# Optimization experiments

Hardware: AMD Instinct MI355X
Metric: run time of the kernel (lower is better)

Reference implementation:

```python
import jax, jax.numpy as jnp
import numpy as np

D_IN = 1024
D_OUT = 1024
SEQ = 4096


def setup_inputs() -> dict:
    key = jax.random.key(0)
    k0, k1, k2, k3 = jax.random.split(key, 4)
    inputs = jax.random.normal(k0, (SEQ, D_IN), dtype=jnp.float32)
    # original uses torch.rand (uniform [0,1)) for weights
    W_q = jax.random.uniform(k1, (D_IN, D_OUT), dtype=jnp.float32)
    W_k = jax.random.uniform(k2, (D_IN, D_OUT), dtype=jnp.float32)
    W_v = jax.random.uniform(k3, (D_IN, D_OUT), dtype=jnp.float32)
    return {"inputs": inputs, "W_q": W_q, "W_k": W_k, "W_v": W_v}


def reference(inputs, W_q, W_k, W_v):
    queries = inputs @ W_q            # [S, d_out]
    keys = inputs @ W_k               # [S, d_out]
    values = inputs @ W_v             # [S, d_out]
    d_k = keys.shape[-1]
    scale = 1.0 / jnp.sqrt(jnp.asarray(d_k, dtype=queries.dtype))
    attn_scores = queries @ keys.T    # [S, S]
    attn_weights = jax.nn.softmax(attn_scores * scale, axis=-1)
    context_vectors = attn_weights @ values  # [S, d_out]
    return context_vectors
```

## Files before the change

kernel.cpp:

```cpp
#include <hip/hip_runtime.h>

typedef unsigned short u16;
typedef __attribute__((ext_vector_type(8))) short bf16x8;
typedef __attribute__((ext_vector_type(4))) float f32x4;

#define SEQ 4096
#define DIM 1024

__device__ __forceinline__ u16 f2bf(float f) {
  unsigned u = __float_as_uint(f);
  return (u16)((u + 0x7fffu + ((u >> 16) & 1u)) >> 16);
}
__device__ __forceinline__ float bf2f(u16 h) {
  return __uint_as_float(((unsigned)h) << 16);
}

__device__ __forceinline__ void gload_lds16(const void* g, void* l) {
  __builtin_amdgcn_global_load_lds(
      (const __attribute__((address_space(1))) void*)g,
      (__attribute__((address_space(3))) void*)l, 16, 0, 0);
}

__device__ __forceinline__ size_t pkoff(int row, int col, int kd) {
  int tile = (row >> 7) * (kd >> 5) + (col >> 5);
  int r7 = row & 127, c5 = col & 31;
  int slot = ((r7 >> 4) << 6) | ((c5 >> 3) << 4) | (r7 & 15);
  return (size_t)tile * 4096 + (size_t)(slot * 8 + (c5 & 7));
}

__device__ __forceinline__ void stage_tile_pk(const u16* __restrict__ g,
                                              u16* lds, int tid) {
  const int w = tid >> 6;
  gload_lds16(g + (size_t)tid * 8, lds + (size_t)(w * 64) * 8);
  gload_lds16(g + (size_t)(256 + tid) * 8, lds + (size_t)(256 + w * 64) * 8);
}

__device__ __forceinline__ void gemm3_db(
    const u16* A0, const u16* A1, const u16* B0, const u16* B1,
    int nkb, u16* lds, f32x4 (&acc)[4][4]) {
  const int tid = threadIdx.x;
  const int w = tid >> 6, l = tid & 63;
  const int wm = w >> 1, wn = w & 1;

#pragma unroll
  for (int mi = 0; mi < 4; ++mi)
#pragma unroll
    for (int ni = 0; ni < 4; ++ni)
      acc[mi][ni] = (f32x4){0.f, 0.f, 0.f, 0.f};

  const int ao = wm * 2048 + l * 8;
  const int bo = wn * 2048 + l * 8;

  stage_tile_pk(A0, lds, tid);
  stage_tile_pk(B0, lds + 4096, tid);
  stage_tile_pk(A1, lds + 8192, tid);
  stage_tile_pk(B1, lds + 12288, tid);

  for (int kb = 0; kb < nkb; ++kb) {
    __syncthreads();
    if (kb + 1 < nkb) {
      u16* nb = lds + ((kb + 1) & 1) * 16384;
      const size_t off = (size_t)(kb + 1) * 4096;
      stage_tile_pk(A0 + off, nb, tid);
      stage_tile_pk(B0 + off, nb + 4096, tid);
      stage_tile_pk(A1 + off, nb + 8192, tid);
      stage_tile_pk(B1 + off, nb + 12288, tid);
    }
    const u16* cb = lds + (kb & 1) * 16384;
    const u16* lA0 = cb;
    const u16* lB0 = cb + 4096;
    const u16* lA1 = cb + 8192;
    const u16* lB1 = cb + 12288;

    bf16x8 a0[4], b0[4];
#pragma unroll
    for (int i = 0; i < 4; ++i) {
      a0[i] = *(const bf16x8*)(lA0 + ao + i * 512);
      b0[i] = *(const bf16x8*)(lB0 + bo + i * 512);
    }
#pragma unroll
    for (int mi = 0; mi < 4; ++mi)
#pragma unroll
      for (int ni = 0; ni < 4; ++ni)
        acc[mi][ni] = __builtin_amdgcn_mfma_f32_16x16x32_bf16(
            a0[mi], b0[ni], acc[mi][ni], 0, 0, 0);
    bf16x8 b1[4];
#pragma unroll
    for (int i = 0; i < 4; ++i) b1[i] = *(const bf16x8*)(lB1 + bo + i * 512);
#pragma unroll
    for (int mi = 0; mi < 4; ++mi)
#pragma unroll
      for (int ni = 0; ni < 4; ++ni)
        acc[mi][ni] = __builtin_amdgcn_mfma_f32_16x16x32_bf16(
            a0[mi], b1[ni], acc[mi][ni], 0, 0, 0);
    bf16x8 a1[4];
#pragma unroll
    for (int i = 0; i < 4; ++i) a1[i] = *(const bf16x8*)(lA1 + ao + i * 512);
#pragma unroll
    for (int mi = 0; mi < 4; ++mi)
#pragma unroll
      for (int ni = 0; ni < 4; ++ni)
        acc[mi][ni] = __builtin_amdgcn_mfma_f32_16x16x32_bf16(
            a1[mi], b0[ni], acc[mi][ni], 0, 0, 0);
  }
  __syncthreads();
}

__device__ __forceinline__ void gemm1_db(
    const u16* A, const u16* B, int nkb, u16* lds, f32x4 (&acc)[4][4]) {
  const int tid = threadIdx.x;
  const int w = tid >> 6, l = tid & 63;
  const int wm = w >> 1, wn = w & 1;

#pragma unroll
  for (int mi = 0; mi < 4; ++mi)
#pragma unroll
    for (int ni = 0; ni < 4; ++ni)
      acc[mi][ni] = (f32x4){0.f, 0.f, 0.f, 0.f};

  const int ao = wm * 2048 + l * 8;
  const int bo = wn * 2048 + l * 8;
  const int nit = nkb >> 1;

  stage_tile_pk(A, lds, tid);
  stage_tile_pk(A + 4096, lds + 4096, tid);
  stage_tile_pk(B, lds + 8192, tid);
  stage_tile_pk(B + 4096, lds + 12288, tid);

  for (int it = 0; it < nit; ++it) {
    __syncthreads();
    if (it + 1 < nit) {
      u16* nb = lds + ((it + 1) & 1) * 16384;
      const size_t off = (size_t)(it + 1) * 8192;
      stage_tile_pk(A + off, nb, tid);
      stage_tile_pk(A + off + 4096, nb + 4096, tid);
      stage_tile_pk(B + off, nb + 8192, tid);
      stage_tile_pk(B + off + 4096, nb + 12288, tid);
    }
    const u16* cb = lds + (it & 1) * 16384;
#pragma unroll
    for (int ht = 0; ht < 2; ++ht) {
      bf16x8 av[4], bv[4];
#pragma unroll
      for (int i = 0; i < 4; ++i) {
        av[i] = *(const bf16x8*)(cb + ht * 4096 + ao + i * 512);
        bv[i] = *(const bf16x8*)(cb + 8192 + ht * 4096 + bo + i * 512);
      }
#pragma unroll
      for (int mi = 0; mi < 4; ++mi)
#pragma unroll
        for (int ni = 0; ni < 4; ++ni)
          acc[mi][ni] = __builtin_amdgcn_mfma_f32_16x16x32_bf16(
              av[mi], bv[ni], acc[mi][ni], 0, 0, 0);
    }
  }
  __syncthreads();
}

#define EPILOGUE_IDX                                          \
  const int tid = threadIdx.x, w = tid >> 6, l = tid & 63;    \
  const int wm = w >> 1, wn = w & 1, lr = l & 15, q = l >> 4; \
  (void)tid;

__device__ __forceinline__ void epilogue_pack(
    f32x4 (&acc)[4][4], u16* lds, int row0, int col0, int kd,
    u16* __restrict__ H, u16* __restrict__ L) {
  const int tid = threadIdx.x, w = tid >> 6, l = tid & 63;
  const int wm = w >> 1, wn = w & 1, lr = l & 15, q = l >> 4;
  float* lC = (float*)lds;
#pragma unroll
  for (int hh = 0; hh < 2; ++hh) {
    if (wm == hh) {
#pragma unroll
      for (int mi = 0; mi < 4; ++mi)
#pragma unroll
        for (int ni = 0; ni < 4; ++ni)
#pragma unroll
          for (int r = 0; r < 4; ++r)
            lC[(mi * 16 + q * 4 + r) * 132 + wn * 64 + ni * 16 + lr] =
                acc[mi][ni][r];
    }
    __syncthreads();
#pragma unroll
    for (int j = 0; j < 2; ++j) {
      int c = tid + 256 * j;
      int row = c >> 3, c0 = (c & 7) * 16;
      u16 hbuf[16], lbuf[16];
#pragma unroll
      for (int i = 0; i < 16; ++i) {
        float v = lC[row * 132 + c0 + i];
        u16 hv = f2bf(v);
        hbuf[i] = hv;
        lbuf[i] = f2bf(v - bf2f(hv));
      }
      int rg = row0 + hh * 64 + row;
      size_t o0 = pkoff(rg, col0 + c0, kd);
      size_t o1 = pkoff(rg, col0 + c0 + 8, kd);
      *(bf16x8*)(H + o0) = *(bf16x8*)(hbuf);
      *(bf16x8*)(H + o1) = *(bf16x8*)(hbuf + 8);
      if (L) {
        *(bf16x8*)(L + o0) = *(bf16x8*)(lbuf);
        *(bf16x8*)(L + o1) = *(bf16x8*)(lbuf + 8);
      }
    }
    if (hh == 0) __syncthreads();
  }
}


__global__ __launch_bounds__(256) void prep_kernel(
    const float* __restrict__ X,
    const float* __restrict__ W0, const float* __restrict__ W1, const float* __restrict__ W2,
    u16* __restrict__ Xh, u16* __restrict__ Xl,
    u16* __restrict__ H0, u16* __restrict__ L0,
    u16* __restrict__ H1, u16* __restrict__ L1,
    u16* __restrict__ H2) {
  const int z = blockIdx.z;
  const int tx = threadIdx.x, ty = threadIdx.y;
  if (z == 0) {
    int idx = (blockIdx.y * 32 + blockIdx.x) * 256 + ty * 32 + tx;
    int row = idx >> 6;
    int c0 = (idx & 63) * 16;
    u16 h[16], lo[16];
#pragma unroll
    for (int j = 0; j < 4; ++j) {
      float4 x = *(const float4*)(X + (size_t)row * DIM + c0 + j * 4);
      float v;
      v = x.x; h[j*4+0] = f2bf(v); lo[j*4+0] = f2bf(v - bf2f(h[j*4+0]));
      v = x.y; h[j*4+1] = f2bf(v); lo[j*4+1] = f2bf(v - bf2f(h[j*4+1]));
      v = x.z; h[j*4+2] = f2bf(v); lo[j*4+2] = f2bf(v - bf2f(h[j*4+2]));
      v = x.w; h[j*4+3] = f2bf(v); lo[j*4+3] = f2bf(v - bf2f(h[j*4+3]));
    }
    size_t o0 = pkoff(row, c0, DIM);
    size_t o1 = pkoff(row, c0 + 8, DIM);
    *(bf16x8*)(Xh + o0) = *(bf16x8*)(h);
    *(bf16x8*)(Xl + o0) = *(bf16x8*)(lo);
    *(bf16x8*)(Xh + o1) = *(bf16x8*)(h + 8);
    *(bf16x8*)(Xl + o1) = *(bf16x8*)(lo + 8);
    return;
  }
  __shared__ float t[32][33];
  const float* W = (z == 1) ? W0 : (z == 2) ? W1 : W2;
  u16* H = (z == 1) ? H0 : (z == 2) ? H1 : H2;
  u16* L = (z == 1) ? L0 : (z == 2) ? L1 : nullptr;
  const int i0 = blockIdx.y * 32, o0 = blockIdx.x * 32;
#pragma unroll
  for (int m = 0; m < 4; ++m)
    t[ty + 8 * m][tx] = W[(size_t)(i0 + ty + 8 * m) * DIM + o0 + tx];
  __syncthreads();
#pragma unroll
  for (int m = 0; m < 4; ++m) {
    float v = t[tx][ty + 8 * m];
    u16 h = f2bf(v);
    size_t o = pkoff(o0 + ty + 8 * m, i0 + tx, DIM);
    H[o] = h;
    if (L) L[o] = f2bf(v - bf2f(h));
  }
}

__global__ __launch_bounds__(256) void qkv_kernel(
    const u16* __restrict__ Xh, const u16* __restrict__ Xl,
    const u16* __restrict__ Wh0, const u16* __restrict__ Wl0,
    const u16* __restrict__ Wh1, const u16* __restrict__ Wl1,
    const u16* __restrict__ Wh2,
    u16* __restrict__ Qh, u16* __restrict__ Ql,
    u16* __restrict__ Kh, u16* __restrict__ Kl,
    u16* __restrict__ VT) {
  __shared__ __align__(16) u16 lds[2 * 4 * 4096];
  const int z = blockIdx.z;
  const int bid = blockIdx.y * 8 + blockIdx.x;
  const int xcd = bid & 7, c = bid >> 3;
  const int Y = xcd * 4 + (c >> 3);
  const int X = c & 7;
  f32x4 acc[4][4];
  if (z < 2) {
    const u16* Wh = z ? Wh1 : Wh0;
    const u16* Wl = z ? Wl1 : Wl0;
    const int row0 = Y * 128, col0 = X * 128;
    gemm3_db(Xh + (size_t)row0 * DIM, Xl + (size_t)row0 * DIM,
             Wh + (size_t)col0 * DIM, Wl + (size_t)col0 * DIM,
             DIM / 32, lds, acc);
    epilogue_pack(acc, lds, row0, col0, DIM, z ? Kh : Qh, z ? Kl : Ql);
  } else {
    const int row0 = X * 128;
    const int col0 = Y * 128;
    gemm1_db(Wh2 + (size_t)row0 * DIM, Xh + (size_t)col0 * DIM,
             DIM / 32, lds, acc);
    epilogue_pack(acc, lds, row0, col0, SEQ, VT, nullptr);
  }
}

__global__ __launch_bounds__(256) void s_kernel(
    const u16* __restrict__ Qh, const u16* __restrict__ Ql,
    const u16* __restrict__ Kh, const u16* __restrict__ Kl,
    float* __restrict__ S) {
  __shared__ __align__(16) u16 lds[2 * 4 * 4096];
  const int bid = blockIdx.y * 32 + blockIdx.x;
  const int xcd = bid & 7, c = bid >> 3;
  const int Y = (xcd & 3) * 8 + (c >> 4);
  const int X = (xcd >> 2) * 16 + (c & 15);
  const int row0 = Y * 128, col0 = X * 128;
  f32x4 acc[4][4];
  gemm3_db(Qh + (size_t)row0 * DIM, Ql + (size_t)row0 * DIM,
           Kh + (size_t)col0 * DIM, Kl + (size_t)col0 * DIM,
           DIM / 32, lds, acc);
  EPILOGUE_IDX
  const float scale = 0.03125f;
#pragma unroll
  for (int mi = 0; mi < 4; ++mi)
#pragma unroll
    for (int ni = 0; ni < 4; ++ni)
#pragma unroll
      for (int r = 0; r < 4; ++r) {
        int row = row0 + wm * 64 + mi * 16 + q * 4 + r;
        int col = col0 + wn * 64 + ni * 16 + lr;
        S[(size_t)row * SEQ + col] = acc[mi][ni][r] * scale;
      }
}

__global__ __launch_bounds__(256) void softmax_kernel(const float* __restrict__ S,
                                                      u16* __restrict__ P) {
  const int row = blockIdx.x;
  const float* s = S + (size_t)row * SEQ;
  const int tid = threadIdx.x;
  const int c0 = tid * 16;
  float v[16];
  float mx = -3.4e38f;
#pragma unroll
  for (int j = 0; j < 4; ++j) {
    float4 x = *(const float4*)(s + c0 + j * 4);
    v[j * 4 + 0] = x.x; v[j * 4 + 1] = x.y; v[j * 4 + 2] = x.z; v[j * 4 + 3] = x.w;
    mx = fmaxf(mx, fmaxf(fmaxf(x.x, x.y), fmaxf(x.z, x.w)));
  }
#pragma unroll
  for (int off = 32; off; off >>= 1) mx = fmaxf(mx, __shfl_xor(mx, off));
  __shared__ float red[8];
  const int w = tid >> 6, l = tid & 63;
  if (l == 0) red[w] = mx;
  __syncthreads();
  mx = fmaxf(fmaxf(red[0], red[1]), fmaxf(red[2], red[3]));
  float sum = 0.f;
#pragma unroll
  for (int i = 0; i < 16; ++i) {
    v[i] = __expf(v[i] - mx);
    sum += v[i];
  }
#pragma unroll
  for (int off = 32; off; off >>= 1) sum += __shfl_xor(sum, off);
  if (l == 0) red[4 + w] = sum;
  __syncthreads();
  sum = red[4] + red[5] + red[6] + red[7];
  const float inv = 1.f / sum;
  u16 p[16];
#pragma unroll
  for (int i = 0; i < 16; ++i) p[i] = f2bf(v[i] * inv);
  *(bf16x8*)(P + pkoff(row, c0, SEQ)) = *(bf16x8*)(p);
  *(bf16x8*)(P + pkoff(row, c0 + 8, SEQ)) = *(bf16x8*)(p + 8);
}

__global__ __launch_bounds__(256) void o_kernel(const u16* __restrict__ P,
                                                const u16* __restrict__ VT,
                                                float* __restrict__ Opart) {
  __shared__ __align__(16) u16 lds[2 * 4 * 4096];
  const int z = blockIdx.z;
  const int bid = blockIdx.y * 8 + blockIdx.x;
  const int xcd = bid & 7, c = bid >> 3;
  const int Y = xcd * 4 + (c >> 3);
  const int X = c & 7;
  const int row0 = Y * 128, col0 = X * 128;
  const u16* A = P + (size_t)row0 * SEQ + (size_t)z * 64 * 4096;
  const u16* B = VT + (size_t)col0 * SEQ + (size_t)z * 64 * 4096;
  f32x4 acc[4][4];
  gemm1_db(A, B, 64, lds, acc);
  EPILOGUE_IDX
  float* O = Opart + (size_t)z * SEQ * DIM;
#pragma unroll
  for (int mi = 0; mi < 4; ++mi)
#pragma unroll
    for (int ni = 0; ni < 4; ++ni)
#pragma unroll
      for (int r = 0; r < 4; ++r) {
        int row = row0 + wm * 64 + mi * 16 + q * 4 + r;
        int col = col0 + wn * 64 + ni * 16 + lr;
        O[(size_t)row * DIM + col] = acc[mi][ni][r];
      }
}

__global__ __launch_bounds__(256) void o_reduce_kernel(const float* __restrict__ Op,
                                                       float* __restrict__ O) {
  const size_t N = (size_t)SEQ * DIM;
  size_t i = ((size_t)blockIdx.x * 256 + threadIdx.x) * 4;
  float4 a = *(const float4*)(Op + i);
  float4 b = *(const float4*)(Op + N + i);
  float4 rr;
  rr.x = a.x + b.x;
  rr.y = a.y + b.y;
  rr.z = a.z + b.z;
  rr.w = a.w + b.w;
  *(float4*)(O + i) = rr;
}

extern "C" void kernel_launch(void* const* d_in, const int* in_sizes, int n_in,
                              void* d_out, int out_size, void* d_ws, size_t ws_size,
                              hipStream_t stream) {
  const float* X = (const float*)d_in[0];
  const float* Wq = (const float*)d_in[1];
  const float* Wk = (const float*)d_in[2];
  const float* Wv = (const float*)d_in[3];

  const size_t MB = 1024 * 1024;
  char* w = (char*)d_ws;
  u16* Xh = (u16*)(w + 0 * MB);
  u16* Xl = (u16*)(w + 8 * MB);
  u16* WqhT = (u16*)(w + 16 * MB);
  u16* WqlT = (u16*)(w + 18 * MB);
  u16* WkhT = (u16*)(w + 20 * MB);
  u16* WklT = (u16*)(w + 22 * MB);
  u16* WvhT = (u16*)(w + 24 * MB);
  u16* Qh = (u16*)(w + 26 * MB);
  u16* Ql = (u16*)(w + 34 * MB);
  u16* Kh = (u16*)(w + 42 * MB);
  u16* Kl = (u16*)(w + 50 * MB);
  u16* VT = (u16*)(w + 58 * MB);
  float* S = (float*)(w + 66 * MB);
  u16* P = (u16*)(w + 26 * MB);
  float* Opart = (float*)(w + 66 * MB);

  prep_kernel<<<dim3(32, 32, 4), dim3(32, 8), 0, stream>>>(
      X, Wq, Wk, Wv, Xh, Xl, WqhT, WqlT, WkhT, WklT, WvhT);
  qkv_kernel<<<dim3(DIM / 128, SEQ / 128, 3), 256, 0, stream>>>(
      Xh, Xl, WqhT, WqlT, WkhT, WklT, WvhT, Qh, Ql, Kh, Kl, VT);
  s_kernel<<<dim3(SEQ / 128, SEQ / 128), 256, 0, stream>>>(Qh, Ql, Kh, Kl, S);
  softmax_kernel<<<SEQ, 256, 0, stream>>>(S, P);
  o_kernel<<<dim3(DIM / 128, SEQ / 128, 2), 256, 0, stream>>>(P, VT, Opart);
  o_reduce_kernel<<<(SEQ * DIM) / (256 * 4), 256, 0, stream>>>(Opart, (float*)d_out);
}
```

Baseline: 302.9 us.

## Use 256x256 tiles with 512 threads and staged pipeline in S GEMM

Replaces the 128x128 split-bf16 QK^T GEMM with a 256x256 tile computed by 8 waves. Each K-step is split into three phases (hi*hi, hi*lo, lo*hi), each guarded by an explicit vmcnt wait and barrier, with prefetch of the next step interleaved between phases. The aim is to raise arithmetic intensity per loaded byte and hide global-to-LDS latency. The cost is 128 KB of LDS per block, higher register pressure from the 8x4 accumulators, and a grid of only 256 blocks.

```diff
diff --git a/kernel.cpp b/kernel.cpp
--- a/kernel.cpp
+++ b/kernel.cpp
@@ -20,6 +20,12 @@
       (const __attribute__((address_space(1))) void*)g,
       (__attribute__((address_space(3))) void*)l, 16, 0, 0);
 }
+
+#define VM0 asm volatile("s_waitcnt vmcnt(0)" ::: "memory")
+#define VM2 asm volatile("s_waitcnt vmcnt(2)" ::: "memory")
+#define VM4 asm volatile("s_waitcnt vmcnt(4)" ::: "memory")
+#define VM6 asm volatile("s_waitcnt vmcnt(6)" ::: "memory")
+#define BAR __builtin_amdgcn_s_barrier()
 
 __device__ __forceinline__ size_t pkoff(int row, int col, int kd) {
   int tile = (row >> 7) * (kd >> 5) + (col >> 5);
@@ -33,6 +39,98 @@
   const int w = tid >> 6;
   gload_lds16(g + (size_t)tid * 8, lds + (size_t)(w * 64) * 8);
   gload_lds16(g + (size_t)(256 + tid) * 8, lds + (size_t)(256 + w * 64) * 8);
+}
+
+__device__ __forceinline__ void stage_q512(const u16* __restrict__ g,
+                                           int kb, int nkb, u16* ldsq, int tid) {
+  const int w = tid >> 6;
+  gload_lds16(g + (size_t)kb * 4096 + tid * 8, ldsq + w * 512);
+  gload_lds16(g + ((size_t)nkb + kb) * 4096 + tid * 8, ldsq + 4096 + w * 512);
+}
+
+__device__ __forceinline__ void gemm3_256(
+    const u16* __restrict__ A0, const u16* __restrict__ A1,
+    const u16* __restrict__ B0, const u16* __restrict__ B1,
+    int nkb, u16* lds, f32x4 (&acc)[8][4]) {
+  const int tid = threadIdx.x;
+  const int w = tid >> 6, l = tid & 63;
+  const int wm = w >> 2, wn = w & 3;
+
+#pragma unroll
+  for (int mi = 0; mi < 8; ++mi)
+#pragma unroll
+    for (int ni = 0; ni < 4; ++ni)
+      acc[mi][ni] = (f32x4){0.f, 0.f, 0.f, 0.f};
+
+  const int QA0 = 0, QA1 = 8192, QB0 = 16384, QB1 = 24576;
+  const int aoff = wm * 4096 + l * 8;
+  const int boff = ((wn & 2) >> 1) * 4096 + (wn & 1) * 2048 + l * 8;
+
+  stage_q512(A0, 0, nkb, lds + QA0, tid);
+  stage_q512(B0, 0, nkb, lds + QB0, tid);
+  stage_q512(B1, 0, nkb, lds + QB1, tid);
+  stage_q512(A1, 0, nkb, lds + QA1, tid);
+
+  for (int kb = 0; kb < nkb; ++kb) {
+    u16* cur = lds + (kb & 1) * 32768;
+    u16* nxt = lds + ((kb + 1) & 1) * 32768;
+    const bool pf = (kb + 1 < nkb);
+    bf16x8 a0[8], b0[4];
+
+    VM4;
+    BAR;
+    if (pf) {
+      stage_q512(A0, kb + 1, nkb, nxt + QA0, tid);
+      stage_q512(B0, kb + 1, nkb, nxt + QB0, tid);
+    }
+#pragma unroll
+    for (int i = 0; i < 8; ++i) a0[i] = *(const bf16x8*)(cur + QA0 + aoff + i * 512);
+#pragma unroll
+    for (int i = 0; i < 4; ++i) b0[i] = *(const bf16x8*)(cur + QB0 + boff + i * 512);
+    __builtin_amdgcn_s_setprio(1);
+#pragma unroll
+    for (int mi = 0; mi < 8; ++mi)
+#pragma unroll
+      for (int ni = 0; ni < 4; ++ni)
+        acc[mi][ni] = __builtin_amdgcn_mfma_f32_16x16x32_bf16(
+            a0[mi], b0[ni], acc[mi][ni], 0, 0, 0);
+    __builtin_amdgcn_s_setprio(0);
+
+    if (pf) { VM6; } else { VM2; }
+    BAR;
+    if (pf) stage_q512(B1, kb + 1, nkb, nxt + QB1, tid);
+    {
+      bf16x8 b1[4];
+#pragma unroll
+      for (int i = 0; i < 4; ++i) b1[i] = *(const bf16x8*)(cur + QB1 + boff + i * 512);
+      __builtin_amdgcn_s_setprio(1);
+#pragma unroll
+      for (int mi = 0; mi < 8; ++mi)
+#pragma unroll
+        for (int ni = 0; ni < 4; ++ni)
+          acc[mi][ni] = __builtin_amdgcn_mfma_f32_16x16x32_bf16(
+              a0[mi], b1[ni], acc[mi][ni], 0, 0, 0);
+      __builtin_amdgcn_s_setprio(0);
+    }
+
+    if (pf) { VM6; } else { VM0; }
+    BAR;
+    if (pf) stage_q512(A1, kb + 1, nkb, nxt + QA1, tid);
+    {
+      bf16x8 a1[8];
+#pragma unroll
+      for (int i = 0; i < 8; ++i) a1[i] = *(const bf16x8*)(cur + QA1 + aoff + i * 512);
+      __builtin_amdgcn_s_setprio(1);
+#pragma unroll
+      for (int mi = 0; mi < 8; ++mi)
+#pragma unroll
+        for (int ni = 0; ni < 4; ++ni)
+          acc[mi][ni] = __builtin_amdgcn_mfma_f32_16x16x32_bf16(
+              a1[mi], b0[ni], acc[mi][ni], 0, 0, 0);
+      __builtin_amdgcn_s_setprio(0);
+    }
+  }
+  __syncthreads();
 }
 
 __device__ __forceinline__ void gemm3_db(
@@ -290,29 +388,30 @@
   }
 }
 
-__global__ __launch_bounds__(256) void s_kernel(
+__global__ __launch_bounds__(512, 2) void s_kernel(
     const u16* __restrict__ Qh, const u16* __restrict__ Ql,
     const u16* __restrict__ Kh, const u16* __restrict__ Kl,
     float* __restrict__ S) {
-  __shared__ __align__(16) u16 lds[2 * 4 * 4096];
-  const int bid = blockIdx.y * 32 + blockIdx.x;
+  __shared__ __align__(16) u16 lds[2 * 32768];
+  const int bid = blockIdx.y * 16 + blockIdx.x;
   const int xcd = bid & 7, c = bid >> 3;
-  const int Y = (xcd & 3) * 8 + (c >> 4);
-  const int X = (xcd >> 2) * 16 + (c & 15);
-  const int row0 = Y * 128, col0 = X * 128;
-  f32x4 acc[4][4];
-  gemm3_db(Qh + (size_t)row0 * DIM, Ql + (size_t)row0 * DIM,
-           Kh + (size_t)col0 * DIM, Kl + (size_t)col0 * DIM,
-           DIM / 32, lds, acc);
-  EPILOGUE_IDX
+  const int Y = (xcd & 3) * 4 + (c >> 3);
+  const int X = (xcd >> 2) * 8 + (c & 7);
+  const int row0 = Y * 256, col0 = X * 256;
+  f32x4 acc[8][4];
+  gemm3_256(Qh + (size_t)row0 * DIM, Ql + (size_t)row0 * DIM,
+            Kh + (size_t)col0 * DIM, Kl + (size_t)col0 * DIM,
+            DIM / 32, lds, acc);
+  const int tid = threadIdx.x, w = tid >> 6, l = tid & 63;
+  const int wm = w >> 2, wn = w & 3, lr = l & 15, q = l >> 4;
   const float scale = 0.03125f;
 #pragma unroll
-  for (int mi = 0; mi < 4; ++mi)
+  for (int mi = 0; mi < 8; ++mi)
 #pragma unroll
     for (int ni = 0; ni < 4; ++ni)
 #pragma unroll
       for (int r = 0; r < 4; ++r) {
-        int row = row0 + wm * 64 + mi * 16 + q * 4 + r;
+        int row = row0 + wm * 128 + mi * 16 + q * 4 + r;
         int col = col0 + wn * 64 + ni * 16 + lr;
         S[(size_t)row * SEQ + col] = acc[mi][ni][r] * scale;
       }
@@ -430,7 +529,7 @@
       X, Wq, Wk, Wv, Xh, Xl, WqhT, WqlT, WkhT, WklT, WvhT);
   qkv_kernel<<<dim3(DIM / 128, SEQ / 128, 3), 256, 0, stream>>>(
       Xh, Xl, WqhT, WqlT, WkhT, WklT, WvhT, Qh, Ql, Kh, Kl, VT);
-  s_kernel<<<dim3(SEQ / 128, SEQ / 128), 256, 0, stream>>>(Qh, Ql, Kh, Kl, S);
+  s_kernel<<<dim3(SEQ / 256, SEQ / 256), 512, 0, stream>>>(Qh, Ql, Kh, Kl, S);
   softmax_kernel<<<SEQ, 256, 0, stream>>>(S, P);
   o_kernel<<<dim3(DIM / 128, SEQ / 128, 2), 256, 0, stream>>>(P, VT, Opart);
   o_reduce_kernel<<<(SEQ * DIM) / (256 * 4), 256, 0, stream>>>(Opart, (float*)d_out);
```

Measured after the change: 299.9 us. About the same (-1.0%).
